# Kernel tuning notes

Measured on AMD Instinct MI355X. Metric: run time of the kernel, lower is better.

The kernel has to match this reference:

```python
import jax, jax.numpy as jnp
import numpy as np

B, H, W, CIN = 4, 56, 56, 64
FILTERS, NDG, KS = 64, 4, 3
FIG = FILTERS // NDG  # filters per deformable group
K = KS * KS           # kernel taps
PAD = (KS - 1) // 2   # 'same' padding for stride 1, dilation 1


def setup_inputs() -> dict:
    key = jax.random.key(0)
    k1, k2, k3, k4 = jax.random.split(key, 4)
    x = jax.random.normal(k1, (B, H, W, CIN), jnp.float32)
    offset_kernel = jax.random.normal(k2, (KS, KS, CIN, K * NDG * 2), jnp.float32) * 0.01
    offset_bias = jax.random.normal(k3, (K * NDG * 2,), jnp.float32) * 0.1
    kernel = jax.random.normal(k4, (KS, KS, FILTERS, CIN), jnp.float32) * (1.0 / np.sqrt(K * CIN))
    return {"x": x, "offset_kernel": offset_kernel, "offset_bias": offset_bias, "kernel": kernel}


def reference(x, offset_kernel, offset_bias, kernel):
    # 1) offset prediction conv (SAME padding, stride 1, dilation 1)
    offset = jax.lax.conv_general_dilated(
        x, offset_kernel, window_strides=(1, 1), padding='SAME',
        dimension_numbers=('NHWC', 'HWIO', 'NHWC')) + offset_bias
    out_h, out_w = offset.shape[1], offset.shape[2]
    # 2) pad input exactly like the layer's _pad_input for 'same'
    xp = jnp.pad(x, ((0, 0), (PAD, PAD), (PAD, PAD), (0, 0)))
    in_h, in_w = xp.shape[1], xp.shape[2]
    # 3) offsets -> [B, oh, ow, K*NDG], channel order (tap k, group g)
    offset = offset.reshape(B, out_h, out_w, K * NDG, 2)
    y_off, x_off = offset[..., 0], offset[..., 1]
    # 4) base conv sampling grid in padded coords (stride=1, dilation=1)
    oh = jnp.arange(out_h)
    ow = jnp.arange(out_w)
    ki = jnp.arange(KS)
    kj = jnp.arange(KS)
    y_base = jnp.broadcast_to(oh[:, None, None, None] + ki[None, None, :, None],
                              (out_h, out_w, KS, KS)).reshape(out_h, out_w, K)
    x_base = jnp.broadcast_to(ow[None, :, None, None] + kj[None, None, None, :],
                              (out_h, out_w, KS, KS)).reshape(out_h, out_w, K)
    # tile over deformable groups: index layout k*NDG + g
    y_base = jnp.repeat(y_base, NDG, axis=-1).astype(jnp.float32)  # [oh,ow,K*NDG]
    x_base = jnp.repeat(x_base, NDG, axis=-1).astype(jnp.float32)
    y = jnp.clip(y_base[None] + y_off, 0.0, in_h - 1)
    xc = jnp.clip(x_base[None] + x_off, 0.0, in_w - 1)
    y0 = jnp.floor(y).astype(jnp.int32)
    x0 = jnp.floor(xc).astype(jnp.int32)
    y1 = jnp.clip(y0 + 1, 0, in_h - 1)
    x1 = jnp.clip(x1_ := x0 + 1, 0, in_w - 1)
    y0 = jnp.clip(y0, 0, in_h - 1)
    x0 = jnp.clip(x0, 0, in_w - 1)

    def gather(yy, xx):  # [B,oh,ow,K*NDG] int -> [B,oh,ow,K*NDG,CIN]
        return jax.vmap(lambda img, a, b: img[a, b])(xp, yy, xx)

    p0 = gather(y0, x0)
    p1 = gather(y0, x1)
    p2 = gather(y1, x0)
    p3 = gather(y1, x1)
    y0f, y1f = y0.astype(jnp.float32), y1.astype(jnp.float32)
    x0f, x1f = x0.astype(jnp.float32), x1.astype(jnp.float32)
    w0 = ((y1f - y) * (x1f - xc))[..., None]
    w1 = ((y1f - y) * (xc - x0f))[..., None]
    w2 = ((y - y0f) * (x1f - xc))[..., None]
    w3 = ((y - y0f) * (xc - x0f))[..., None]
    pixels = w0 * p0 + w1 * p1 + w2 * p2 + w3 * p3  # [B,oh,ow,K*NDG,CIN]
    pixels = pixels.reshape(B, out_h, out_w, KS, KS, NDG, CIN)
    # 5) grouped combination: filter f = g*FIG + r uses group g; sum over taps and Cin
    kW = kernel.reshape(KS, KS, NDG, FIG, CIN)
    out = jnp.einsum('bhwijgc,ijgfc->bhwgf', pixels, kW)
    return out.reshape(B, out_h, out_w, FILTERS)
```

## Files before the change

### kernel.cpp

```cpp
#include <hip/hip_runtime.h>


#define NH 56
#define NW 56
#define NC 64
#define NDG 4
#define NK 9
#define NOFF 72
#define NOFFP 80
#define NF 64
#define KTOT 576
#define HWPIX 3136
#define NPIX 12544

#define PW    14
#define WR    5
#define WC    18
#define WPOS  (WR * WC)
#define NBLK  (4 * NH * 4)

#define WS_OFFKT 0
#define WS_WK    92160

typedef _Float16 half8   __attribute__((ext_vector_type(8)));
typedef _Float16 half4   __attribute__((ext_vector_type(4)));
typedef float    floatx4 __attribute__((ext_vector_type(4)));

__global__ __launch_bounds__(256)
void dcn_prep(const float* __restrict__ offk,
              const float* __restrict__ wk,
              _Float16* __restrict__ offkt,
              _Float16* __restrict__ wkh)
{
    const int i = blockIdx.x * 256 + threadIdx.x;
    if (i < NOFFP * KTOT) {
        const int oc = i / KTOT;
        const int kk = i - oc * KTOT;
        const float v = (oc < NOFF) ? offk[kk * NOFF + oc] : 0.0f;
        offkt[i] = (_Float16)v;
    }
    const int j = i - NOFFP * KTOT;
    if (j >= 0 && j < NK * NF * NC) wkh[j] = (_Float16)wk[j];
}

__device__ __forceinline__ int winh_idx(int pos, int c) {
    return (pos << 6) + (c ^ ((pos & 7) << 3));
}

__global__ __launch_bounds__(256, 4)
void dcn_main(const float* __restrict__ x,
              const _Float16* __restrict__ offkt,
              const float* __restrict__ offb,
              const _Float16* __restrict__ wkh,
              float* __restrict__ out)
{
    __shared__ __align__(16) _Float16 s_winh[WPOS * NC];
    __shared__ float s_off[PW * NOFF];
    __shared__ __align__(16) float s_cww[36 * 16 * 4];
    __shared__ __align__(8)  unsigned s_cwl[36 * 16 * 2];
    __shared__ unsigned s_cwf[36 * 16];

    const int tid  = threadIdx.x;
    const int w    = tid >> 6;
    const int lane = tid & 63;
    const int m    = lane & 15;
    const int kq   = lane >> 4;
    const int kq8  = kq * 8;

    const int blk = blockIdx.x;
    const int b   = blk / (NH * 4);
    const int r2  = blk - b * (NH * 4);
    const int oh  = r2 >> 2;
    const int ow0 = (r2 & 3) * PW;
    const int bb  = b * HWPIX;

    for (int i = tid; i < WPOS * 16; i += 256) {
        const int pos = i >> 4;
        const int g4  = (i & 15) * 4;
        const int ry  = pos / WC;
        const int rx  = pos - ry * WC;
        const int iy  = oh + ry - 2;
        const int ix  = ow0 + rx - 2;
        float4 v = make_float4(0.f, 0.f, 0.f, 0.f);
        if ((unsigned)iy < NH && (unsigned)ix < NW)
            v = *(const float4*)&x[(size_t)((bb + iy * NW + ix) * NC) + g4];
        half4 h;
        h[0] = (_Float16)v.x; h[1] = (_Float16)v.y;
        h[2] = (_Float16)v.z; h[3] = (_Float16)v.w;
        *(half4*)&s_winh[winh_idx(pos, g4)] = h;
    }
    __syncthreads();

    const int oc0 = w * 16 + m;
    floatx4 acc0, acc1;
    { const float bv = offb[oc0]; acc0 = (floatx4){bv, bv, bv, bv}; }
    { const float bv = (w == 3 && m < 8) ? offb[64 + m] : 0.0f;
      acc1 = (floatx4){bv, bv, bv, bv}; }

    #pragma unroll
    for (int k = 0; k < NK; ++k) {
        const int ki = k / 3, kj = k - 3 * ki;
        const int pos = (ki + 1) * WC + (m + kj + 1);
        #pragma unroll
        for (int s = 0; s < 2; ++s) {
            const half8 af = *(const half8*)&s_winh[winh_idx(pos, s * 32 + kq8)];
            const int kkb = k * 64 + s * 32 + kq8;
            const half8 bf0 = *(const half8*)&offkt[(size_t)oc0 * KTOT + kkb];
            acc0 = __builtin_amdgcn_mfma_f32_16x16x32_f16(af, bf0, acc0, 0, 0, 0);
            if (w == 3) {
                const half8 bf1 = *(const half8*)&offkt[(size_t)(64 + m) * KTOT + kkb];
                acc1 = __builtin_amdgcn_mfma_f32_16x16x32_f16(af, bf1, acc1, 0, 0, 0);
            }
        }
    }
    #pragma unroll
    for (int r = 0; r < 4; ++r)
        if (kq * 4 + r < PW)
            s_off[(kq * 4 + r) * NOFF + oc0] = acc0[r];
    if (w == 3 && m < 8) {
        #pragma unroll
        for (int r = 0; r < 4; ++r)
            if (kq * 4 + r < PW)
                s_off[(kq * 4 + r) * NOFF + 64 + m] = acc1[r];
    }
    __syncthreads();

    for (int i = tid; i < 36 * 16; i += 256) {
        const int kg = i >> 4;
        const int p  = i & 15;
        float4 wv = make_float4(0.f, 0.f, 0.f, 0.f);
        unsigned c0 = 0, c1 = 0, cfv = 0;
        if (p < PW) {
            const int k  = kg >> 2;
            const int ki = k / 3, kj = k - 3 * ki;
            const int ow = ow0 + p;
            const float offy = s_off[p * NOFF + kg * 2 + 0];
            const float offx = s_off[p * NOFF + kg * 2 + 1];
            float yv = fminf(fmaxf((float)(oh + ki) + offy, 0.0f), 57.0f);
            float xv = fminf(fmaxf((float)(ow + kj) + offx, 0.0f), 57.0f);
            const float y0f = floorf(yv), x0f = floorf(xv);
            const int y0 = (int)y0f, x0 = (int)x0f;
            const int y1 = min(y0 + 1, 57), x1 = min(x0 + 1, 57);
            const float ly = yv - y0f,       lx = xv - x0f;
            const float hy = (float)y1 - yv, hx = (float)x1 - xv;
            const bool vy0 = (unsigned)(y0 - 1) < NH;
            const bool vy1 = (unsigned)(y1 - 1) < NH;
            const bool vx0 = (unsigned)(x0 - 1) < NW;
            const bool vx1 = (unsigned)(x1 - 1) < NW;
            wv = make_float4((vy0 && vx0) ? hy * hx : 0.0f,
                             (vy0 && vx1) ? hy * lx : 0.0f,
                             (vy1 && vx0) ? ly * hx : 0.0f,
                             (vy1 && vx1) ? ly * lx : 0.0f);
            const int y0c = min(max(y0 - 1, 0), NH - 1);
            const int y1c = min(max(y1 - 1, 0), NH - 1);
            const int x0c = min(max(x0 - 1, 0), NW - 1);
            const int x1c = min(max(x1 - 1, 0), NW - 1);
            const int ry0 = y0c - oh + 2, ry1 = y1c - oh + 2;
            const int rx0 = x0c - ow0 + 2, rx1 = x1c - ow0 + 2;
            if ((unsigned)ry0 < WR && (unsigned)ry1 < WR &&
                (unsigned)rx0 < WC && (unsigned)rx1 < WC) {
                c0 = (unsigned)(ry0 * WC + rx0) | ((unsigned)(ry0 * WC + rx1) << 16);
                c1 = (unsigned)(ry1 * WC + rx0) | ((unsigned)(ry1 * WC + rx1) << 16);
            } else {
                cfv = 0x80000000u | ((unsigned)y0c << 18) | ((unsigned)x0c << 12)
                    | ((unsigned)y1c << 6) | (unsigned)x1c;
            }
        }
        *(float4*)&s_cww[i * 4] = wv;
        s_cwl[i * 2 + 0] = c0;
        s_cwl[i * 2 + 1] = c1;
        s_cwf[i] = cfv;
    }
    __syncthreads();

    floatx4 accB = (floatx4){0.f, 0.f, 0.f, 0.f};
    const int tb = w * 16 + m;
    #pragma unroll
    for (int k = 0; k < NK; ++k) {
        const int sl = k * 64 + tb;
        const float4   cw = *(const float4*)&s_cww[sl * 4];
        const unsigned c0 = s_cwl[sl * 2 + 0];
        const unsigned c1 = s_cwl[sl * 2 + 1];
        const unsigned cf = s_cwf[sl];

        const _Float16* wp = &wkh[(size_t)(k * NF + w * 16 + m) * NC];
        const half8 bf0 = *(const half8*)&wp[kq8];
        const half8 bf1 = *(const half8*)&wp[32 + kq8];

        const int p00 = c0 & 0xFFFF, p01 = c0 >> 16;
        const int p10 = c1 & 0xFFFF, p11 = c1 >> 16;
        const int ca = kq8, cb = 32 + kq8;
        const half8 q00a = *(const half8*)&s_winh[winh_idx(p00, ca)];
        const half8 q01a = *(const half8*)&s_winh[winh_idx(p01, ca)];
        const half8 q10a = *(const half8*)&s_winh[winh_idx(p10, ca)];
        const half8 q11a = *(const half8*)&s_winh[winh_idx(p11, ca)];
        const half8 q00b = *(const half8*)&s_winh[winh_idx(p00, cb)];
        const half8 q01b = *(const half8*)&s_winh[winh_idx(p01, cb)];
        const half8 q10b = *(const half8*)&s_winh[winh_idx(p10, cb)];
        const half8 q11b = *(const half8*)&s_winh[winh_idx(p11, cb)];

        half8 af0, af1;
        #pragma unroll
        for (int j = 0; j < 8; ++j) {
            float v0 = cw.x * (float)q00a[j];
            v0 = fmaf(cw.y, (float)q01a[j], v0);
            v0 = fmaf(cw.z, (float)q10a[j], v0);
            v0 = fmaf(cw.w, (float)q11a[j], v0);
            af0[j] = (_Float16)v0;
            float v1 = cw.x * (float)q00b[j];
            v1 = fmaf(cw.y, (float)q01b[j], v1);
            v1 = fmaf(cw.z, (float)q10b[j], v1);
            v1 = fmaf(cw.w, (float)q11b[j], v1);
            af1[j] = (_Float16)v1;
        }

        if (__builtin_expect(cf != 0, 0)) {
            const int y0c = (cf >> 18) & 63, x0c = (cf >> 12) & 63;
            const int y1c = (cf >> 6) & 63,  x1c = cf & 63;
            const int i00 = (bb + y0c * NW + x0c) * NC;
            const int i01 = (bb + y0c * NW + x1c) * NC;
            const int i10 = (bb + y1c * NW + x0c) * NC;
            const int i11 = (bb + y1c * NW + x1c) * NC;
            #pragma unroll
            for (int j = 0; j < 8; ++j) {
                float v0 = cw.x * (float)(_Float16)x[i00 + kq8 + j];
                v0 = fmaf(cw.y, (float)(_Float16)x[i01 + kq8 + j], v0);
                v0 = fmaf(cw.z, (float)(_Float16)x[i10 + kq8 + j], v0);
                v0 = fmaf(cw.w, (float)(_Float16)x[i11 + kq8 + j], v0);
                af0[j] = (_Float16)v0;
                float v1 = cw.x * (float)(_Float16)x[i00 + 32 + kq8 + j];
                v1 = fmaf(cw.y, (float)(_Float16)x[i01 + 32 + kq8 + j], v1);
                v1 = fmaf(cw.z, (float)(_Float16)x[i10 + 32 + kq8 + j], v1);
                v1 = fmaf(cw.w, (float)(_Float16)x[i11 + 32 + kq8 + j], v1);
                af1[j] = (_Float16)v1;
            }
        }

        accB = __builtin_amdgcn_mfma_f32_16x16x32_f16(af0, bf0, accB, 0, 0, 0);
        accB = __builtin_amdgcn_mfma_f32_16x16x32_f16(af1, bf1, accB, 0, 0, 0);
    }

    #pragma unroll
    for (int r = 0; r < 4; ++r) {
        const int row = kq * 4 + r;
        if (row < PW)
            out[(size_t)(bb + oh * NW + ow0 + row) * NF + w * 16 + m] = accB[r];
    }
}

extern "C" void kernel_launch(void* const* d_in, const int* in_sizes, int n_in,
                              void* d_out, int out_size, void* d_ws, size_t ws_size,
                              hipStream_t stream) {
    const float* xin  = (const float*)d_in[0];
    const float* offk = (const float*)d_in[1];
    const float* offb = (const float*)d_in[2];
    const float* wk   = (const float*)d_in[3];
    float* outp = (float*)d_out;

    _Float16* offkt = (_Float16*)((char*)d_ws + WS_OFFKT);
    _Float16* wkh   = (_Float16*)((char*)d_ws + WS_WK);

    dcn_prep<<<324, 256, 0, stream>>>(offk, wk, offkt, wkh);
    dcn_main<<<NBLK, 256, 0, stream>>>(xin, offkt, offb, wkh, outp);
}
```

Baseline: 85.52 us.

## Retile output block from 1x14 row strip to 2x8 pixel tile

Each block now covers a 2x8 patch of output pixels instead of 14 pixels in one row. All 16 MFMA rows do useful work, where before two of them were padding, and the grid becomes 4*28*7 blocks. The shared input window changes from 5x18 to 6x12 positions, so the halo is taller but narrower. That changes how often deformed samples land outside the window and fall back to global memory.

```diff
diff --git a/kernel.cpp b/kernel.cpp
--- a/kernel.cpp
+++ b/kernel.cpp
@@ -13,11 +13,12 @@
 #define HWPIX 3136
 #define NPIX 12544
 
-#define PW    14
-#define WR    5
-#define WC    18
+#define PR    2
+#define PC    8
+#define WR    6
+#define WC    12
 #define WPOS  (WR * WC)
-#define NBLK  (4 * NH * 4)
+#define NBLK  (4 * (NH / PR) * (NW / PC))
 
 #define WS_OFFKT 0
 #define WS_WK    92160
@@ -55,7 +56,7 @@
               float* __restrict__ out)
 {
     __shared__ __align__(16) _Float16 s_winh[WPOS * NC];
-    __shared__ float s_off[PW * NOFF];
+    __shared__ float s_off[16 * NOFF];
     __shared__ __align__(16) float s_cww[36 * 16 * 4];
     __shared__ __align__(8)  unsigned s_cwl[36 * 16 * 2];
     __shared__ unsigned s_cwf[36 * 16];
@@ -68,10 +69,10 @@
     const int kq8  = kq * 8;
 
     const int blk = blockIdx.x;
-    const int b   = blk / (NH * 4);
-    const int r2  = blk - b * (NH * 4);
-    const int oh  = r2 >> 2;
-    const int ow0 = (r2 & 3) * PW;
+    const int b   = blk / ((NH / PR) * (NW / PC));
+    const int r2  = blk - b * ((NH / PR) * (NW / PC));
+    const int oh  = (r2 / (NW / PC)) * PR;
+    const int ow0 = (r2 - (r2 / (NW / PC)) * (NW / PC)) * PC;
     const int bb  = b * HWPIX;
 
     for (int i = tid; i < WPOS * 16; i += 256) {
@@ -100,7 +101,7 @@
     #pragma unroll
     for (int k = 0; k < NK; ++k) {
         const int ki = k / 3, kj = k - 3 * ki;
-        const int pos = (ki + 1) * WC + (m + kj + 1);
+        const int pos = (ki + 1 + (m >> 3)) * WC + ((m & 7) + kj + 1);
         #pragma unroll
         for (int s = 0; s < 2; ++s) {
             const half8 af = *(const half8*)&s_winh[winh_idx(pos, s * 32 + kq8)];
@@ -115,56 +116,52 @@
     }
     #pragma unroll
     for (int r = 0; r < 4; ++r)
-        if (kq * 4 + r < PW)
-            s_off[(kq * 4 + r) * NOFF + oc0] = acc0[r];
+        s_off[(kq * 4 + r) * NOFF + oc0] = acc0[r];
     if (w == 3 && m < 8) {
         #pragma unroll
         for (int r = 0; r < 4; ++r)
-            if (kq * 4 + r < PW)
-                s_off[(kq * 4 + r) * NOFF + 64 + m] = acc1[r];
+            s_off[(kq * 4 + r) * NOFF + 64 + m] = acc1[r];
     }
     __syncthreads();
 
     for (int i = tid; i < 36 * 16; i += 256) {
         const int kg = i >> 4;
         const int p  = i & 15;
-        float4 wv = make_float4(0.f, 0.f, 0.f, 0.f);
+        const int k  = kg >> 2;
+        const int ki = k / 3, kj = k - 3 * ki;
+        const int ohp = oh + (p >> 3);
+        const int owp = ow0 + (p & 7);
+        const float offy = s_off[p * NOFF + kg * 2 + 0];
+        const float offx = s_off[p * NOFF + kg * 2 + 1];
+        float yv = fminf(fmaxf((float)(ohp + ki) + offy, 0.0f), 57.0f);
+        float xv = fminf(fmaxf((float)(owp + kj) + offx, 0.0f), 57.0f);
+        const float y0f = floorf(yv), x0f = floorf(xv);
+        const int y0 = (int)y0f, x0 = (int)x0f;
+        const int y1 = min(y0 + 1, 57), x1 = min(x0 + 1, 57);
+        const float ly = yv - y0f,       lx = xv - x0f;
+        const float hy = (float)y1 - yv, hx = (float)x1 - xv;
+        const bool vy0 = (unsigned)(y0 - 1) < NH;
+        const bool vy1 = (unsigned)(y1 - 1) < NH;
+        const bool vx0 = (unsigned)(x0 - 1) < NW;
+        const bool vx1 = (unsigned)(x1 - 1) < NW;
+        const float4 wv = make_float4((vy0 && vx0) ? hy * hx : 0.0f,
+                                      (vy0 && vx1) ? hy * lx : 0.0f,
+                                      (vy1 && vx0) ? ly * hx : 0.0f,
+                                      (vy1 && vx1) ? ly * lx : 0.0f);
+        const int y0c = min(max(y0 - 1, 0), NH - 1);
+        const int y1c = min(max(y1 - 1, 0), NH - 1);
+        const int x0c = min(max(x0 - 1, 0), NW - 1);
+        const int x1c = min(max(x1 - 1, 0), NW - 1);
+        const int ry0 = y0c - oh + 2, ry1 = y1c - oh + 2;
+        const int rx0 = x0c - ow0 + 2, rx1 = x1c - ow0 + 2;
         unsigned c0 = 0, c1 = 0, cfv = 0;
-        if (p < PW) {
-            const int k  = kg >> 2;
-            const int ki = k / 3, kj = k - 3 * ki;
-            const int ow = ow0 + p;
-            const float offy = s_off[p * NOFF + kg * 2 + 0];
-            const float offx = s_off[p * NOFF + kg * 2 + 1];
-            float yv = fminf(fmaxf((float)(oh + ki) + offy, 0.0f), 57.0f);
-            float xv = fminf(fmaxf((float)(ow + kj) + offx, 0.0f), 57.0f);
-            const float y0f = floorf(yv), x0f = floorf(xv);
-            const int y0 = (int)y0f, x0 = (int)x0f;
-            const int y1 = min(y0 + 1, 57), x1 = min(x0 + 1, 57);
-            const float ly = yv - y0f,       lx = xv - x0f;
-            const float hy = (float)y1 - yv, hx = (float)x1 - xv;
-            const bool vy0 = (unsigned)(y0 - 1) < NH;
-            const bool vy1 = (unsigned)(y1 - 1) < NH;
-            const bool vx0 = (unsigned)(x0 - 1) < NW;
-            const bool vx1 = (unsigned)(x1 - 1) < NW;
-            wv = make_float4((vy0 && vx0) ? hy * hx : 0.0f,
-                             (vy0 && vx1) ? hy * lx : 0.0f,
-                             (vy1 && vx0) ? ly * hx : 0.0f,
-                             (vy1 && vx1) ? ly * lx : 0.0f);
-            const int y0c = min(max(y0 - 1, 0), NH - 1);
-            const int y1c = min(max(y1 - 1, 0), NH - 1);
-            const int x0c = min(max(x0 - 1, 0), NW - 1);
-            const int x1c = min(max(x1 - 1, 0), NW - 1);
-            const int ry0 = y0c - oh + 2, ry1 = y1c - oh + 2;
-            const int rx0 = x0c - ow0 + 2, rx1 = x1c - ow0 + 2;
-            if ((unsigned)ry0 < WR && (unsigned)ry1 < WR &&
-                (unsigned)rx0 < WC && (unsigned)rx1 < WC) {
-                c0 = (unsigned)(ry0 * WC + rx0) | ((unsigned)(ry0 * WC + rx1) << 16);
-                c1 = (unsigned)(ry1 * WC + rx0) | ((unsigned)(ry1 * WC + rx1) << 16);
-            } else {
-                cfv = 0x80000000u | ((unsigned)y0c << 18) | ((unsigned)x0c << 12)
-                    | ((unsigned)y1c << 6) | (unsigned)x1c;
-            }
+        if ((unsigned)ry0 < WR && (unsigned)ry1 < WR &&
+            (unsigned)rx0 < WC && (unsigned)rx1 < WC) {
+            c0 = (unsigned)(ry0 * WC + rx0) | ((unsigned)(ry0 * WC + rx1) << 16);
+            c1 = (unsigned)(ry1 * WC + rx0) | ((unsigned)(ry1 * WC + rx1) << 16);
+        } else {
+            cfv = 0x80000000u | ((unsigned)y0c << 18) | ((unsigned)x0c << 12)
+                | ((unsigned)y1c << 6) | (unsigned)x1c;
         }
         *(float4*)&s_cww[i * 4] = wv;
         s_cwl[i * 2 + 0] = c0;
@@ -243,8 +240,8 @@
     #pragma unroll
     for (int r = 0; r < 4; ++r) {
         const int row = kq * 4 + r;
-        if (row < PW)
-            out[(size_t)(bb + oh * NW + ow0 + row) * NF + w * 16 + m] = accB[r];
+        out[(size_t)(bb + (oh + (row >> 3)) * NW + ow0 + (row & 7)) * NF
+            + w * 16 + m] = accB[r];
     }
 }
 
```

Result: no change. 84.99 us (-0.6%).
